# Optimization experiments

Measured on AMD Instinct MI355X. Metric: run time of the kernel, lower is better.

## Reference

```python
import jax, jax.numpy as jnp
import numpy as np

B, D = 4096, 1024
TEMPERATURE = 0.07


def setup_inputs() -> dict:
    key = jax.random.key(0)
    k1, k2, k3, k4, k5, k6 = jax.random.split(key, 6)
    return {
        "mri_features": jax.random.normal(k1, (B, D), dtype=jnp.float32),
        "pet_features": jax.random.normal(k2, (B, D), dtype=jnp.float32),
        "labels": jax.random.randint(k3, (B,), 0, 3, dtype=jnp.int64),
        "subtype_mri": jax.random.randint(k4, (B,), 0, 4, dtype=jnp.int64),
        "subtype_pet": jax.random.randint(k5, (B,), 0, 4, dtype=jnp.int64),
        "clinical_similarity": jax.random.uniform(k6, (B, B), dtype=jnp.float32),
    }


def _build_weights(labels, subtype_mri, subtype_pet, clinical_similarity):
    # vectorized form of the O(B^2) python loop
    same_label = labels[:, None] == labels[None, :]
    label_zero = labels[:, None] == 0
    sub_match = (subtype_mri[:, None] == subtype_mri[None, :]) & (
        subtype_pet[:, None] == subtype_pet[None, :]
    )
    n = labels.shape[0]
    not_diag = ~jnp.eye(n, dtype=bool)
    mask = same_label & (label_zero | sub_match) & not_diag
    weights = jnp.where(mask, clinical_similarity, 0.0)
    row_sums = weights.sum(axis=1, keepdims=True)
    row_sums = jnp.where(row_sums == 0, 1.0, row_sums)
    return weights / row_sums


def _contrastive(fi, fj, weights):
    fi = fi / jnp.linalg.norm(fi, axis=1, keepdims=True)
    fj = fj / jnp.linalg.norm(fj, axis=1, keepdims=True)
    sim = jnp.matmul(fi, fj.T) / TEMPERATURE  # [B, B]
    log_sm = jax.nn.log_softmax(sim, axis=1)
    return -jnp.sum(weights * log_sm) / fi.shape[0]


def reference(mri_features, pet_features, labels, subtype_mri, subtype_pet, clinical_similarity):
    weights = _build_weights(labels, subtype_mri, subtype_pet, clinical_similarity)
    pairs = [
        (mri_features, pet_features),
        (pet_features, mri_features),
        (mri_features, mri_features),
        (pet_features, pet_features),
    ]
    total = 0.0
    for fi, fj in pairs:
        total = total + _contrastive(fi, fj, weights)
    return total / len(pairs)
```

## Files before the change

kernel.cpp:

```cpp
#include <hip/hip_runtime.h>
#include <hip/hip_bf16.h>
#include <hip/hip_fp8.h>
#include <math.h>

typedef __attribute__((ext_vector_type(4))) float f32x4;

#define NB 4096
#define ND 1024
#define INV_T 14.2857142857142857f

__device__ inline float fp82f(unsigned char b) {
    __hip_fp8_e4m3 h; h.__x = b;
    return (float)h;
}
__device__ inline void gload16(const void* g, void* l) {
    __builtin_amdgcn_global_load_lds(
        (const __attribute__((address_space(1))) void*)g,
        (__attribute__((address_space(3))) void*)l, 16, 0, 0);
}

__global__ __launch_bounds__(256) void norm_kernel(
        const float* __restrict__ M, const float* __restrict__ P,
        unsigned char* __restrict__ Mf, unsigned char* __restrict__ Pf) {
    int row = blockIdx.x & (NB - 1);
    const float* src = (blockIdx.x < NB) ? M : P;
    unsigned char* dst = (blockIdx.x < NB) ? Mf : Pf;
    int tid = threadIdx.x;
    float4 v = ((const float4*)(src + (size_t)row * ND))[tid];
    float ss = v.x * v.x + v.y * v.y + v.z * v.z + v.w * v.w;
    for (int off = 32; off; off >>= 1) ss += __shfl_down(ss, off);
    __shared__ float red[4];
    int lane = tid & 63, w = tid >> 6;
    if (lane == 0) red[w] = ss;
    __syncthreads();
    float rn = rsqrtf(red[0] + red[1] + red[2] + red[3]);
    int p = __builtin_amdgcn_cvt_pk_fp8_f32(v.x * rn, v.y * rn, 0, false);
    p = __builtin_amdgcn_cvt_pk_fp8_f32(v.z * rn, v.w * rn, p, true);
    ((int*)dst)[row * 256 + tid] = p;
}

__global__ __launch_bounds__(256) void key_kernel(
        const int* __restrict__ labels, const int* __restrict__ sm,
        const int* __restrict__ sp, int* __restrict__ code) {
    int i = blockIdx.x * 256 + threadIdx.x;
    if (i < NB) {
        int l = labels[i];
        code[i] = (l == 0) ? 0x40000000 : (1 + l + (sm[i] << 8) + (sp[i] << 16));
    }
}

__global__ __launch_bounds__(256) void rowsumw_kernel(
        const float* __restrict__ cs, const int* __restrict__ code,
        unsigned char* __restrict__ W, float* __restrict__ flag) {
    int i = blockIdx.x;
    int ci = code[i];
    int tid = threadIdx.x;
    const float4* row = (const float4*)(cs + (size_t)i * NB);
    const int4* c4 = (const int4*)code;
    float4 v[4];
    int4 cj[4];
    float s = 0.f;
#pragma unroll
    for (int k = 0; k < 4; ++k) {
        int t = tid + k * 256;
        v[k] = row[t];
        cj[k] = c4[t];
        int j = t * 4;
        if (cj[k].x == ci && j + 0 != i) s += v[k].x;
        if (cj[k].y == ci && j + 1 != i) s += v[k].y;
        if (cj[k].z == ci && j + 2 != i) s += v[k].z;
        if (cj[k].w == ci && j + 3 != i) s += v[k].w;
    }
    for (int off = 1; off < 64; off <<= 1) s += __shfl_xor(s, off);
    __shared__ float red[4];
    int lane = tid & 63, w = tid >> 6;
    if (lane == 0) red[w] = s;
    __syncthreads();
    float tot = red[0] + red[1] + red[2] + red[3];
    float inv = (tot > 0.f) ? 1.f / tot : 0.f;
#pragma unroll
    for (int k = 0; k < 4; ++k) {
        int t = tid + k * 256;
        int j = t * 4;
        float f0 = (cj[k].x == ci && j + 0 != i) ? v[k].x * inv : 0.f;
        float f1 = (cj[k].y == ci && j + 1 != i) ? v[k].y * inv : 0.f;
        float f2 = (cj[k].z == ci && j + 2 != i) ? v[k].z * inv : 0.f;
        float f3 = (cj[k].w == ci && j + 3 != i) ? v[k].w * inv : 0.f;
        int p = __builtin_amdgcn_cvt_pk_fp8_f32(f0, f1, 0, false);
        p = __builtin_amdgcn_cvt_pk_fp8_f32(f2, f3, p, true);
        ((int*)W)[((size_t)i * NB + j) >> 2] = p;
    }
    if (tid == 0) flag[i] = (tot > 0.f) ? 1.f : 0.f;
}

__global__ __launch_bounds__(256) void symw_kernel(unsigned char* __restrict__ W) {
    __shared__ unsigned char Ta[64][80], Tb[64][80];
    int b = blockIdx.x;
    int ti = 0, t = b;
    while (t >= 64 - ti) { t -= 64 - ti; ++ti; }
    int tj = ti + t;
    size_t ra = (size_t)ti * 64, rb = (size_t)tj * 64;
    int tid = threadIdx.x;
    int r = tid >> 2, c0 = (tid & 3) * 16;
    int4 a0 = *(const int4*)&W[(ra + r) * NB + rb + c0];
    int4 b0 = *(const int4*)&W[(rb + r) * NB + ra + c0];
    *(int4*)&Ta[r][c0] = a0;
    *(int4*)&Tb[r][c0] = b0;
    __syncthreads();
    unsigned char oa[16], ob[16];
#pragma unroll
    for (int c = 0; c < 16; c += 2) {
        int cc = c0 + c;
        float a_lo = fp82f(Ta[r][cc])     + fp82f(Tb[cc][r]);
        float a_hi = fp82f(Ta[r][cc + 1]) + fp82f(Tb[cc + 1][r]);
        float b_lo = fp82f(Tb[r][cc])     + fp82f(Ta[cc][r]);
        float b_hi = fp82f(Tb[r][cc + 1]) + fp82f(Ta[cc + 1][r]);
        int pa = __builtin_amdgcn_cvt_pk_fp8_f32(a_lo, a_hi, 0, false);
        int pb = __builtin_amdgcn_cvt_pk_fp8_f32(b_lo, b_hi, 0, false);
        oa[c] = (unsigned char)(pa & 0xff); oa[c + 1] = (unsigned char)((pa >> 8) & 0xff);
        ob[c] = (unsigned char)(pb & 0xff); ob[c + 1] = (unsigned char)((pb >> 8) & 0xff);
    }
    *(int4*)&W[(ra + r) * NB + rb + c0] = *(int4*)&oa[0];
    *(int4*)&W[(rb + r) * NB + ra + c0] = *(int4*)&ob[0];
}

__global__ __launch_bounds__(256, 3) void mega_gemm(
        const unsigned char* __restrict__ Mf, const unsigned char* __restrict__ Pf,
        const unsigned char* __restrict__ Wg,
        float* __restrict__ rowsum1, float* __restrict__ colsum1,
        float* __restrict__ rowsum3, float* __restrict__ rowsum4,
        float* __restrict__ dots) {
    __shared__ char smem[49152] __attribute__((aligned(16)));

    int tid = threadIdx.x;
    int lane = tid & 63, w = tid >> 6;
    int wm = w >> 1, wn = w & 1;
    int lr = lane & 15, lg = lane >> 4;

    int b = (blockIdx.x & 7) * 260 + (blockIdx.x >> 3);
    int bi, bj, mode;
    const unsigned char *A, *Bm;
    if (b < 1024) {
        int st = b >> 4;
        int sb = b & 15;
        bi = (st >> 3) * 4 + (sb >> 2);
        bj = (st & 7) * 4 + (sb & 3);
        A = Mf; Bm = Pf; mode = 0;
    } else {
        int s = b - 1024;
        int md = (s >= 528) ? 1 : 0;
        s -= md * 528;
        bi = 0;
        while (s >= 32 - bi) { s -= 32 - bi; ++bi; }
        bj = bi + s;
        A = md ? Pf : Mf; Bm = A;
        mode = 1 + md;
    }
    bool offdiag = (bi != bj);
    size_t rowBase = (size_t)bi * 128;
    size_t colBase = (size_t)bj * 128;
    float* rowTgt = (mode == 0) ? rowsum1 : ((mode == 1) ? rowsum3 : rowsum4);
    float* colTgt = (mode == 0) ? colsum1 : rowTgt;

    int sr = lane >> 2;
    int scs = (lane & 3) ^ (sr & 3) ^ ((sr >> 2) & 3);
    const unsigned char* gA = A + (rowBase + w * 32 + sr) * ND + scs * 16;
    const unsigned char* gB = Bm + (colBase + w * 32 + sr) * ND + scs * 16;

    f32x4 acc[4][4] = {};

#define STAGE(bufi, t) {                                                    \
        int k0_ = (t) * 64;                                                 \
        char* baseA_ = smem + (bufi) * 16384;                               \
        char* baseB_ = baseA_ + 8192;                                       \
        gload16(gA + k0_,                   baseA_ + (w * 2    ) * 1024);   \
        gload16(gA + (size_t)16 * ND + k0_, baseA_ + (w * 2 + 1) * 1024);   \
        gload16(gB + k0_,                   baseB_ + (w * 2    ) * 1024);   \
        gload16(gB + (size_t)16 * ND + k0_, baseB_ + (w * 2 + 1) * 1024);   \
    }
#define COMPUTE(bufi) {                                                     \
        const unsigned char* sA = (const unsigned char*)(smem + (bufi) * 16384); \
        const unsigned char* sB = sA + 8192;                                \
        int rx = (lr & 3) ^ ((lr >> 2) & 3);                                \
        _Pragma("unroll")                                                   \
        for (int ks = 0; ks < 2; ++ks) {                                    \
            int cp = (((ks * 2) + (lg >> 1)) ^ rx) * 16 + (lg & 1) * 8;     \
            long av[4], bv[4];                                              \
            _Pragma("unroll")                                               \
            for (int n = 0; n < 4; ++n)                                     \
                bv[n] = *(const long*)&sB[(wn * 64 + n * 16 + lr) * 64 + cp]; \
            _Pragma("unroll")                                               \
            for (int i = 0; i < 4; ++i)                                     \
                av[i] = *(const long*)&sA[(wm * 64 + i * 16 + lr) * 64 + cp]; \
            _Pragma("unroll")                                               \
            for (int i = 0; i < 4; ++i)                                     \
                _Pragma("unroll")                                           \
                for (int n = 0; n < 4; ++n)                                 \
                    acc[i][n] = __builtin_amdgcn_mfma_f32_16x16x32_fp8_fp8( \
                        av[i], bv[n], acc[i][n], 0, 0, 0);                  \
        }                                                                   \
    }
#define BAR __builtin_amdgcn_s_barrier()

    STAGE(0, 0); STAGE(1, 1);
    asm volatile("s_waitcnt vmcnt(4)" ::: "memory"); BAR;
    for (int t = 0; t < 14; ++t) {
        STAGE((t + 2) % 3, t + 2);
        COMPUTE(t % 3);
        asm volatile("s_waitcnt vmcnt(4)" ::: "memory"); BAR;
    }
    COMPUTE(14 % 3);
    asm volatile("s_waitcnt vmcnt(0)" ::: "memory"); BAR;
    COMPUTE(15 % 3);
    __syncthreads();
#undef STAGE
#undef COMPUTE
#undef BAR

    unsigned char* wl = (unsigned char*)smem;
    float d1 = 0.f;
    float cexp[4] = {0.f, 0.f, 0.f, 0.f};

#pragma unroll
    for (int c = 0; c < 4; ++c) {
        int q = w * 4 + c;
        int sw = 8 * q + (lane >> 3);
        int gchunk = (lane & 7) ^ (sw & 7);
        gload16(Wg + (rowBase + sw) * (size_t)NB + colBase + gchunk * 16,
                smem + q * 1024);
    }
    __syncthreads();
#pragma unroll
    for (int m = 0; m < 4; ++m) {
        float rexp[4] = {0.f, 0.f, 0.f, 0.f};
#pragma unroll
        for (int n = 0; n < 4; ++n) {
            int jl = wn * 64 + n * 16 + lr;
#pragma unroll
            for (int r = 0; r < 4; ++r) {
                int rl = wm * 64 + m * 16 + lg * 4 + r;
                float sim = acc[m][n][r] * INV_T;
                float e = __expf(sim - INV_T);
                rexp[r] += e;
                cexp[n] += e;
                int ck = (jl >> 4) ^ (rl & 7);
                d1 += fp82f(wl[rl * 128 + ck * 16 + (jl & 15)]) * sim;
            }
        }
#pragma unroll
        for (int r = 0; r < 4; ++r) {
            float v = rexp[r];
            v += __shfl_xor(v, 1); v += __shfl_xor(v, 2);
            v += __shfl_xor(v, 4); v += __shfl_xor(v, 8);
            if (lr == 0)
                atomicAdd(&rowTgt[rowBase + wm * 64 + m * 16 + lg * 4 + r], v);
        }
    }

    if (mode == 0 || offdiag) {
#pragma unroll
        for (int n = 0; n < 4; ++n) {
            float v = cexp[n];
            v += __shfl_xor(v, 16); v += __shfl_xor(v, 32);
            if (lg == 0)
                atomicAdd(&colTgt[colBase + wn * 64 + n * 16 + lr], v);
        }
    }

    float dtot = (mode != 0 && !offdiag) ? 0.5f * d1 : d1;
    for (int off = 32; off; off >>= 1) dtot += __shfl_xor(dtot, off);
    if (lane == 0) {
        if (mode == 0) atomicAdd(&dots[0], dtot);
        else           atomicAdd(&dots[1 + mode], dtot);
    }
}

__global__ __launch_bounds__(256) void finalize_kernel(
        const float* __restrict__ rowsum1, const float* __restrict__ colsum1,
        const float* __restrict__ rowsum3, const float* __restrict__ rowsum4,
        const float* __restrict__ flag, const float* __restrict__ dots,
        float* __restrict__ out) {
    int tid = threadIdx.x;
    float l = 0.f;
    for (int i = tid; i < NB; i += 256) {
        if (flag[i] != 0.f) {
            l += 4.f * INV_T + logf(rowsum1[i]) + logf(colsum1[i]) +
                 logf(rowsum3[i]) + logf(rowsum4[i]);
        }
    }
    for (int off = 32; off; off >>= 1) l += __shfl_down(l, off);
    __shared__ float red[4];
    int lane = tid & 63, w = tid >> 6;
    if (lane == 0) red[w] = l;
    __syncthreads();
    if (tid == 0) {
        float L = red[0] + red[1] + red[2] + red[3];
        float dt = dots[0] + dots[1] + dots[2] + dots[3];
        out[0] = (L - dt) / (4.0f * (float)NB);
    }
}

extern "C" void kernel_launch(void* const* d_in, const int* in_sizes, int n_in,
                              void* d_out, int out_size, void* d_ws, size_t ws_size,
                              hipStream_t stream) {
    const float* M = (const float*)d_in[0];
    const float* P = (const float*)d_in[1];
    const int* labels = (const int*)d_in[2];
    const int* sm = (const int*)d_in[3];
    const int* sp = (const int*)d_in[4];
    const float* cs = (const float*)d_in[5];
    float* out = (float*)d_out;

    char* ws = (char*)d_ws;
    unsigned char* Mf = (unsigned char*)ws;
    unsigned char* Pf = (unsigned char*)(ws + (size_t)4 * 1024 * 1024);
    unsigned char* W = (unsigned char*)(ws + (size_t)16 * 1024 * 1024);
    char* p = ws + (size_t)48 * 1024 * 1024;
    int* code = (int*)p;        p += 16384;
    float* flag = (float*)p;    p += 16384;
    float* rowsum1 = (float*)p; p += 16384;
    float* colsum1 = (float*)p; p += 16384;
    float* rowsum3 = (float*)p; p += 16384;
    float* rowsum4 = (float*)p; p += 16384;
    float* dots = (float*)p;

    hipMemsetAsync(rowsum1, 0, 4 * 16384 + 256, stream);

    norm_kernel<<<2 * NB, 256, 0, stream>>>(M, P, Mf, Pf);
    key_kernel<<<NB / 256, 256, 0, stream>>>(labels, sm, sp, code);
    rowsumw_kernel<<<NB, 256, 0, stream>>>(cs, code, W, flag);
    symw_kernel<<<2080, 256, 0, stream>>>(W);

    mega_gemm<<<2080, 256, 0, stream>>>(Mf, Pf, W, rowsum1, colsum1,
                                        rowsum3, rowsum4, dots);

    finalize_kernel<<<1, 256, 0, stream>>>(rowsum1, colsum1, rowsum3, rowsum4,
                                           flag, dots, out);
}
```

Measured before the change: 194.2 us.

## Fuse weight symmetrization into GEMM epilogue and prefetch weight tiles during final k-steps

```diff
diff --git a/kernel.cpp b/kernel.cpp
--- a/kernel.cpp
+++ b/kernel.cpp
@@ -93,43 +93,10 @@
     if (tid == 0) flag[i] = (tot > 0.f) ? 1.f : 0.f;
 }
 
-__global__ __launch_bounds__(256) void symw_kernel(unsigned char* __restrict__ W) {
-    __shared__ unsigned char Ta[64][80], Tb[64][80];
-    int b = blockIdx.x;
-    int ti = 0, t = b;
-    while (t >= 64 - ti) { t -= 64 - ti; ++ti; }
-    int tj = ti + t;
-    size_t ra = (size_t)ti * 64, rb = (size_t)tj * 64;
-    int tid = threadIdx.x;
-    int r = tid >> 2, c0 = (tid & 3) * 16;
-    int4 a0 = *(const int4*)&W[(ra + r) * NB + rb + c0];
-    int4 b0 = *(const int4*)&W[(rb + r) * NB + ra + c0];
-    *(int4*)&Ta[r][c0] = a0;
-    *(int4*)&Tb[r][c0] = b0;
-    __syncthreads();
-    unsigned char oa[16], ob[16];
-#pragma unroll
-    for (int c = 0; c < 16; c += 2) {
-        int cc = c0 + c;
-        float a_lo = fp82f(Ta[r][cc])     + fp82f(Tb[cc][r]);
-        float a_hi = fp82f(Ta[r][cc + 1]) + fp82f(Tb[cc + 1][r]);
-        float b_lo = fp82f(Tb[r][cc])     + fp82f(Ta[cc][r]);
-        float b_hi = fp82f(Tb[r][cc + 1]) + fp82f(Ta[cc + 1][r]);
-        int pa = __builtin_amdgcn_cvt_pk_fp8_f32(a_lo, a_hi, 0, false);
-        int pb = __builtin_amdgcn_cvt_pk_fp8_f32(b_lo, b_hi, 0, false);
-        oa[c] = (unsigned char)(pa & 0xff); oa[c + 1] = (unsigned char)((pa >> 8) & 0xff);
-        ob[c] = (unsigned char)(pb & 0xff); ob[c + 1] = (unsigned char)((pb >> 8) & 0xff);
-    }
-    *(int4*)&W[(ra + r) * NB + rb + c0] = *(int4*)&oa[0];
-    *(int4*)&W[(rb + r) * NB + ra + c0] = *(int4*)&ob[0];
-}
-
 __global__ __launch_bounds__(256, 3) void mega_gemm(
         const unsigned char* __restrict__ Mf, const unsigned char* __restrict__ Pf,
         const unsigned char* __restrict__ Wg,
-        float* __restrict__ rowsum1, float* __restrict__ colsum1,
-        float* __restrict__ rowsum3, float* __restrict__ rowsum4,
-        float* __restrict__ dots) {
+        float* __restrict__ outs) {
     __shared__ char smem[49152] __attribute__((aligned(16)));
 
     int tid = threadIdx.x;
@@ -159,8 +126,9 @@
     bool offdiag = (bi != bj);
     size_t rowBase = (size_t)bi * 128;
     size_t colBase = (size_t)bj * 128;
-    float* rowTgt = (mode == 0) ? rowsum1 : ((mode == 1) ? rowsum3 : rowsum4);
-    float* colTgt = (mode == 0) ? colsum1 : rowTgt;
+    bool needW2 = (rowBase != colBase);
+    float* rowTgt = outs + ((mode == 0) ? 0 : (mode == 1) ? 8192 : 12288);
+    float* colTgt = (mode == 0) ? (outs + 4096) : rowTgt;
 
     int sr = lane >> 2;
     int scs = (lane & 3) ^ (sr & 3) ^ ((sr >> 2) & 3);
@@ -178,11 +146,21 @@
         gload16(gB + k0_,                   baseB_ + (w * 2    ) * 1024);   \
         gload16(gB + (size_t)16 * ND + k0_, baseB_ + (w * 2 + 1) * 1024);   \
     }
+#define STAGEW(dst, rbase, cbase) {                                         \
+        _Pragma("unroll")                                                   \
+        for (int c = 0; c < 4; ++c) {                                       \
+            int q_ = w * 4 + c;                                             \
+            int sw_ = 8 * q_ + (lane >> 3);                                 \
+            int gch_ = (lane & 7) ^ (sw_ & 7);                              \
+            gload16(Wg + ((rbase) + sw_) * (size_t)NB + (cbase) + gch_ * 16,\
+                    (dst) + q_ * 1024);                                     \
+        }                                                                   \
+    }
 #define COMPUTE(bufi) {                                                     \
         const unsigned char* sA = (const unsigned char*)(smem + (bufi) * 16384); \
         const unsigned char* sB = sA + 8192;                                \
         int rx = (lr & 3) ^ ((lr >> 2) & 3);                                \
-        _Pragma("unroll")                                                   \
+        _Pragma("unroll 1")                                                 \
         for (int ks = 0; ks < 2; ++ks) {                                    \
             int cp = (((ks * 2) + (lg >> 1)) ^ rx) * 16 + (lg & 1) * 8;     \
             long av[4], bv[4];                                              \
@@ -209,27 +187,22 @@
         COMPUTE(t % 3);
         asm volatile("s_waitcnt vmcnt(4)" ::: "memory"); BAR;
     }
-    COMPUTE(14 % 3);
+    STAGEW(smem + 16384, rowBase, colBase);
+    COMPUTE(2);
+    BAR;
+    if (needW2) STAGEW(smem + 32768, colBase, rowBase);
     asm volatile("s_waitcnt vmcnt(0)" ::: "memory"); BAR;
-    COMPUTE(15 % 3);
-    __syncthreads();
+    COMPUTE(0);
 #undef STAGE
+#undef STAGEW
 #undef COMPUTE
 #undef BAR
 
-    unsigned char* wl = (unsigned char*)smem;
+    const unsigned char* wl1 = (const unsigned char*)smem + 16384;
+    const unsigned char* wl2 = needW2 ? (const unsigned char*)smem + 32768 : wl1;
     float d1 = 0.f;
     float cexp[4] = {0.f, 0.f, 0.f, 0.f};
 
-#pragma unroll
-    for (int c = 0; c < 4; ++c) {
-        int q = w * 4 + c;
-        int sw = 8 * q + (lane >> 3);
-        int gchunk = (lane & 7) ^ (sw & 7);
-        gload16(Wg + (rowBase + sw) * (size_t)NB + colBase + gchunk * 16,
-                smem + q * 1024);
-    }
-    __syncthreads();
 #pragma unroll
     for (int m = 0; m < 4; ++m) {
         float rexp[4] = {0.f, 0.f, 0.f, 0.f};
@@ -243,8 +216,9 @@
                 float e = __expf(sim - INV_T);
                 rexp[r] += e;
                 cexp[n] += e;
-                int ck = (jl >> 4) ^ (rl & 7);
-                d1 += fp82f(wl[rl * 128 + ck * 16 + (jl & 15)]) * sim;
+                float w1v = fp82f(wl1[rl * 128 + (((jl >> 4) ^ (rl & 7)) << 4) + (jl & 15)]);
+                float w2v = fp82f(wl2[jl * 128 + (((rl >> 4) ^ (jl & 7)) << 4) + (rl & 15)]);
+                d1 += (w1v + w2v) * sim;
             }
         }
 #pragma unroll
@@ -270,16 +244,20 @@
     float dtot = (mode != 0 && !offdiag) ? 0.5f * d1 : d1;
     for (int off = 32; off; off >>= 1) dtot += __shfl_xor(dtot, off);
     if (lane == 0) {
+        float* dots = outs + 16384;
         if (mode == 0) atomicAdd(&dots[0], dtot);
         else           atomicAdd(&dots[1 + mode], dtot);
     }
 }
 
 __global__ __launch_bounds__(256) void finalize_kernel(
-        const float* __restrict__ rowsum1, const float* __restrict__ colsum1,
-        const float* __restrict__ rowsum3, const float* __restrict__ rowsum4,
-        const float* __restrict__ flag, const float* __restrict__ dots,
+        const float* __restrict__ outs, const float* __restrict__ flag,
         float* __restrict__ out) {
+    const float* rowsum1 = outs;
+    const float* colsum1 = outs + 4096;
+    const float* rowsum3 = outs + 8192;
+    const float* rowsum4 = outs + 12288;
+    const float* dots = outs + 16384;
     int tid = threadIdx.x;
     float l = 0.f;
     for (int i = tid; i < NB; i += 256) {
@@ -316,24 +294,17 @@
     unsigned char* Pf = (unsigned char*)(ws + (size_t)4 * 1024 * 1024);
     unsigned char* W = (unsigned char*)(ws + (size_t)16 * 1024 * 1024);
     char* p = ws + (size_t)48 * 1024 * 1024;
-    int* code = (int*)p;        p += 16384;
-    float* flag = (float*)p;    p += 16384;
-    float* rowsum1 = (float*)p; p += 16384;
-    float* colsum1 = (float*)p; p += 16384;
-    float* rowsum3 = (float*)p; p += 16384;
-    float* rowsum4 = (float*)p; p += 16384;
-    float* dots = (float*)p;
-
-    hipMemsetAsync(rowsum1, 0, 4 * 16384 + 256, stream);
+    int* code = (int*)p;    p += 16384;
+    float* flag = (float*)p; p += 16384;
+    float* outs = (float*)p;
+
+    hipMemsetAsync(outs, 0, 4 * 16384 + 256, stream);
 
     norm_kernel<<<2 * NB, 256, 0, stream>>>(M, P, Mf, Pf);
     key_kernel<<<NB / 256, 256, 0, stream>>>(labels, sm, sp, code);
     rowsumw_kernel<<<NB, 256, 0, stream>>>(cs, code, W, flag);
-    symw_kernel<<<2080, 256, 0, stream>>>(W);
-
-    mega_gemm<<<2080, 256, 0, stream>>>(Mf, Pf, W, rowsum1, colsum1,
-                                        rowsum3, rowsum4, dots);
-
-    finalize_kernel<<<1, 256, 0, stream>>>(rowsum1, colsum1, rowsum3, rowsum4,
-                                           flag, dots, out);
-}
+
+    mega_gemm<<<2080, 256, 0, stream>>>(Mf, Pf, W, outs);
+
+    finalize_kernel<<<1, 256, 0, stream>>>(outs, flag, out);
+}
```

Result: no change. 194.2 us (-0.0%).
